# Performance work log

Hardware: AMD Instinct MI355X
Metric: run time of the kernel (lower is better)

The kernel has to match this reference:

```python
import jax, jax.numpy as jnp
import numpy as np

B, S, D = 2, 2048, 2048
NH = 16
HD = D // NH  # 128
MAX_POS = 4096
ROPE_THETA = 10000.0


def rotate_half(x):
    x1, x2 = x[..., : x.shape[-1] // 2], x[..., x.shape[-1] // 2 :]
    return jnp.concatenate((-x2, x1), axis=-1)


def rope_tables(dtype=jnp.float32):
    inv_freq = 1.0 / (ROPE_THETA ** (jnp.arange(0, HD, 2, dtype=jnp.float32) / HD))
    t = jnp.arange(MAX_POS, dtype=jnp.float32)
    freqs = jnp.outer(t, inv_freq)              # [MAX_POS, HD/2]
    emb = jnp.concatenate((freqs, freqs), axis=-1)  # [MAX_POS, HD]
    return jnp.cos(emb).astype(dtype), jnp.sin(emb).astype(dtype)


def setup_inputs() -> dict:
    key = jax.random.key(0)
    ks = jax.random.split(key, 9)
    sc = 0.02
    return {
        "hidden_states": jax.random.normal(ks[0], (B, S, D), jnp.float32),
        "position_ids": jnp.arange(B * S, dtype=jnp.int32).reshape(B, S),
        "Wq": jax.random.normal(ks[1], (D, D), jnp.float32) * sc,
        "bq": jax.random.normal(ks[2], (D,), jnp.float32) * sc,
        "Wk": jax.random.normal(ks[3], (D, D), jnp.float32) * sc,
        "bk": jax.random.normal(ks[4], (D,), jnp.float32) * sc,
        "Wv": jax.random.normal(ks[5], (D, D), jnp.float32) * sc,
        "bv": jax.random.normal(ks[6], (D,), jnp.float32) * sc,
        "Wo": jax.random.normal(ks[7], (D, D), jnp.float32) * sc,
    }


def reference(hidden_states, position_ids, Wq, bq, Wk, bk, Wv, bv, Wo):
    b, s, _ = hidden_states.shape
    # projections (torch Linear: x @ W.T + b)
    q = (hidden_states @ Wq.T + bq).reshape(b, s, NH, HD).transpose(0, 2, 1, 3)
    k = (hidden_states @ Wk.T + bk).reshape(b, s, NH, HD).transpose(0, 2, 1, 3)
    v = (hidden_states @ Wv.T + bv).reshape(b, s, NH, HD).transpose(0, 2, 1, 3)
    # RoPE
    cos_t, sin_t = rope_tables(hidden_states.dtype)
    cos = cos_t[position_ids][:, None, :, :]  # [B,1,S,HD]
    sin = sin_t[position_ids][:, None, :, :]
    q = q * cos + rotate_half(q) * sin
    k = k * cos + rotate_half(k) * sin
    # NOTE: faithful to the source bug — softmax is computed but its result is
    # discarded; the AV matmul uses the UNNORMALIZED scaled scores.
    attn_weights = jnp.einsum("bhqd,bhkd->bhqk", q, k) / (HD ** 0.5)
    _ = jax.nn.softmax(attn_weights.astype(jnp.float32), axis=-1)  # dead, as in source
    attn_output = jnp.einsum("bhqk,bhkd->bhqd", attn_weights, v)
    attn_output = attn_output.transpose(0, 2, 1, 3).reshape(b, s, D)
    return attn_output @ Wo.T
```

## Files before the change

kernel.cpp:

```cpp
#include <hip/hip_runtime.h>
#include <hip/hip_bf16.h>


typedef __attribute__((ext_vector_type(8))) short bf16x8s;
typedef __attribute__((ext_vector_type(4))) float f32x4;

__device__ __forceinline__ ushort f2bf(float f) {
    union { float f; unsigned int u; } x; x.f = f;
    unsigned int u = x.u;
    unsigned int r = (u + 0x7fffu + ((u >> 16) & 1u)) >> 16;
    return (ushort)r;
}

__device__ __forceinline__ void gload_lds16(const void* g, void* l) {
    __builtin_amdgcn_global_load_lds((__attribute__((address_space(1))) const void*)g,
                                     (__attribute__((address_space(3))) void*)l, 16, 0, 0);
}

template<bool BIAS, bool OBF16>
__global__ __launch_bounds__(256)
void gemm_nt(const ushort* __restrict__ A, const ushort* __restrict__ B,
             const float* __restrict__ bias, void* __restrict__ Cv,
             int K, int lda, int ldb, int ldc, int ZH,
             long sAb, long sAh, long sBb, long sBh, long sCb, long sCh)
{
    __shared__ ushort As[128 * 32];
    __shared__ ushort Bs[128 * 32];

    int z  = blockIdx.z;
    int zb = z / ZH, zh = z - zb * ZH;
    const ushort* Ab = A + (size_t)(sAb * zb + sAh * zh);
    const ushort* Bb = B + (size_t)(sBb * zb + sBh * zh);
    size_t Coff = (size_t)(sCb * zb + sCh * zh);

    int m0 = blockIdx.x * 128, n0 = blockIdx.y * 128;
    int t = threadIdx.x;
    int l = t & 63, w = t >> 6;
    int wm = (w >> 1) * 64, wn = (w & 1) * 64;
    int lr = l & 15, lk = (l >> 4) * 8;

    f32x4 acc[4][4];
#pragma unroll
    for (int i = 0; i < 4; i++)
#pragma unroll
        for (int j = 0; j < 4; j++)
            acc[i][j] = (f32x4){0.f, 0.f, 0.f, 0.f};

    int c0 = t, c1 = t + 256;
    int r0 = c0 >> 2, k0c = (c0 & 3) * 8;
    int r1 = c1 >> 2, k1c = (c1 & 3) * 8;

    for (int kt = 0; kt < K; kt += 32) {
        __syncthreads();
        gload_lds16(Ab + (size_t)(m0 + r0) * lda + kt + k0c, &As[c0 * 8]);
        gload_lds16(Ab + (size_t)(m0 + r1) * lda + kt + k1c, &As[c1 * 8]);
        gload_lds16(Bb + (size_t)(n0 + r0) * ldb + kt + k0c, &Bs[c0 * 8]);
        gload_lds16(Bb + (size_t)(n0 + r1) * ldb + kt + k1c, &Bs[c1 * 8]);
        __syncthreads();

        bf16x8s af[4], bf[4];
#pragma unroll
        for (int i = 0; i < 4; i++) {
            af[i] = *(const bf16x8s*)&As[(wm + i * 16 + lr) * 32 + lk];
            bf[i] = *(const bf16x8s*)&Bs[(wn + i * 16 + lr) * 32 + lk];
        }
#pragma unroll
        for (int mi = 0; mi < 4; mi++)
#pragma unroll
            for (int ni = 0; ni < 4; ni++)
                acc[mi][ni] = __builtin_amdgcn_mfma_f32_16x16x32_bf16(
                    af[mi], bf[ni], acc[mi][ni], 0, 0, 0);
    }

    int rr = (l >> 4) * 4;
#pragma unroll
    for (int mi = 0; mi < 4; mi++) {
#pragma unroll
        for (int ni = 0; ni < 4; ni++) {
            int gr = m0 + wm + mi * 16 + rr;
            int gc = n0 + wn + ni * 16 + lr;
            float bv = BIAS ? bias[gc] : 0.f;
#pragma unroll
            for (int r = 0; r < 4; r++) {
                float v = acc[mi][ni][r] + bv;
                size_t off = Coff + (size_t)(gr + r) * ldc + gc;
                if (OBF16) ((ushort*)Cv)[off] = f2bf(v);
                else       ((float*)Cv)[off]  = v;
            }
        }
    }
}

__global__ __launch_bounds__(256)
void rope_qk(const float* __restrict__ Qf, float* __restrict__ Kio,
             const int* __restrict__ pos, ushort* __restrict__ Qb)
{
    int tid = blockIdx.x * 256 + threadIdx.x;
    int row = tid >> 10;
    int r = tid & 1023;
    int h = r >> 6, d = r & 63;
    int p = pos[row];
    float invf = exp2f((float)d * (-13.287712379549449f / 64.0f));
    float ang = (float)p * invf;
    float s, c;
    sincosf(ang, &s, &c);
    size_t base = (size_t)row * 2048 + h * 128 + d;
    float q1 = Qf[base], q2 = Qf[base + 64];
    Qb[base]      = f2bf(q1 * c - q2 * s);
    Qb[base + 64] = f2bf(q2 * c + q1 * s);
    float k1 = Kio[base], k2 = Kio[base + 64];
    Kio[base]      = k1 * c - k2 * s;
    Kio[base + 64] = k2 * c + k1 * s;
}

__global__ __launch_bounds__(256)
void ktv_partial(const float* __restrict__ Kf, const float* __restrict__ Vf,
                 float* __restrict__ part)
{
    int bh = blockIdx.x;
    int b = bh >> 4, h = bh & 15;
    int s0 = blockIdx.y * 128;
    const float* Kp = Kf + ((size_t)(b * 2048 + s0)) * 2048 + h * 128;
    const float* Vp = Vf + ((size_t)(b * 2048 + s0)) * 2048 + h * 128;

    __shared__ float Ks[32][128];
    __shared__ float Vs[32][128];

    int t = threadIdx.x;
    int tx = t & 15, ty = t >> 4;
    float acc[8][8];
#pragma unroll
    for (int i = 0; i < 8; i++)
#pragma unroll
        for (int j = 0; j < 8; j++) acc[i][j] = 0.f;

    for (int sb = 0; sb < 128; sb += 32) {
        __syncthreads();
#pragma unroll
        for (int i = 0; i < 4; i++) {
            int idx = t + i * 256;
            int rw = idx >> 5, c4 = (idx & 31) * 4;
            *(float4*)&Ks[rw][c4] = *(const float4*)&Kp[(size_t)(sb + rw) * 2048 + c4];
            *(float4*)&Vs[rw][c4] = *(const float4*)&Vp[(size_t)(sb + rw) * 2048 + c4];
        }
        __syncthreads();
        for (int ss = 0; ss < 32; ss++) {
            float kv[8], vv[8];
            *(float4*)&kv[0] = *(const float4*)&Ks[ss][tx * 8];
            *(float4*)&kv[4] = *(const float4*)&Ks[ss][tx * 8 + 4];
            *(float4*)&vv[0] = *(const float4*)&Vs[ss][ty * 8];
            *(float4*)&vv[4] = *(const float4*)&Vs[ss][ty * 8 + 4];
#pragma unroll
            for (int i = 0; i < 8; i++)
#pragma unroll
                for (int j = 0; j < 8; j++)
                    acc[i][j] += kv[i] * vv[j];
        }
    }
    float* pp = part + ((size_t)blockIdx.y * 32 + bh) * 16384;
#pragma unroll
    for (int i = 0; i < 8; i++)
#pragma unroll
        for (int j = 0; j < 8; j++)
            pp[(tx * 8 + i) * 128 + (ty * 8 + j)] = acc[i][j];
}

__global__ __launch_bounds__(256)
void reduce_ktv(const float* __restrict__ part, ushort* __restrict__ Mb)
{
    int i = blockIdx.x * 256 + threadIdx.x;
    float s = 0.f;
#pragma unroll
    for (int p = 0; p < 16; p++) s += part[(size_t)p * 524288 + i];
    Mb[i] = f2bf(s * 0.08838834764831845f);
}

__global__ __launch_bounds__(256)
void conv_f32_bf16(const float* __restrict__ in, ushort* __restrict__ out, int n4)
{
    int i = blockIdx.x * 256 + threadIdx.x;
    if (i >= n4) return;
    float4 v = ((const float4*)in)[i];
    ushort4 o;
    o.x = f2bf(v.x); o.y = f2bf(v.y); o.z = f2bf(v.z); o.w = f2bf(v.w);
    ((ushort4*)out)[i] = o;
}

extern "C" void kernel_launch(void* const* d_in, const int* in_sizes, int n_in,
                              void* d_out, int out_size, void* d_ws, size_t ws_size,
                              hipStream_t stream)
{
    const float* hs = (const float*)d_in[0];
    const int*  pos = (const int*)d_in[1];
    const float* Wq = (const float*)d_in[2];
    const float* bq = (const float*)d_in[3];
    const float* Wk = (const float*)d_in[4];
    const float* bk = (const float*)d_in[5];
    const float* Wv = (const float*)d_in[6];
    const float* bv = (const float*)d_in[7];
    const float* Wo = (const float*)d_in[8];
    float* out = (float*)d_out;
    char* ws = (char*)d_ws;

    ushort* HSB  = (ushort*)(ws + 0);
    ushort* WBUF = (ushort*)(ws + 16777216);
    float*  Kf   = (float*)(ws + 25165824);
    float*  Vf   = (float*)(ws + 58720256);
    ushort* QB   = (ushort*)(ws + 92274688);
    ushort* MB   = (ushort*)(ws + 109051904);
    float*  Qf   = out;
    float*  PART = out;
    ushort* NT   = (ushort*)Vf;

    dim3 blk(256);
    dim3 gQKV(32, 16, 1);

    conv_f32_bf16<<<8192, blk, 0, stream>>>(hs, HSB, 2097152);

    conv_f32_bf16<<<4096, blk, 0, stream>>>(Wq, WBUF, 1048576);
    gemm_nt<true, false><<<gQKV, blk, 0, stream>>>(HSB, WBUF, bq, Qf,
        2048, 2048, 2048, 2048, 1, 0, 0, 0, 0, 0, 0);

    conv_f32_bf16<<<4096, blk, 0, stream>>>(Wk, WBUF, 1048576);
    gemm_nt<true, false><<<gQKV, blk, 0, stream>>>(HSB, WBUF, bk, Kf,
        2048, 2048, 2048, 2048, 1, 0, 0, 0, 0, 0, 0);

    conv_f32_bf16<<<4096, blk, 0, stream>>>(Wv, WBUF, 1048576);
    gemm_nt<true, false><<<gQKV, blk, 0, stream>>>(HSB, WBUF, bv, Vf,
        2048, 2048, 2048, 2048, 1, 0, 0, 0, 0, 0, 0);

    rope_qk<<<16384, blk, 0, stream>>>(Qf, Kf, pos, QB);

    ktv_partial<<<dim3(32, 16, 1), blk, 0, stream>>>(Kf, Vf, PART);
    reduce_ktv<<<2048, blk, 0, stream>>>(PART, MB);

    conv_f32_bf16<<<4096, blk, 0, stream>>>(Wo, WBUF, 1048576);

    gemm_nt<false, true><<<dim3(16, 1, 32), blk, 0, stream>>>(WBUF, MB, nullptr, NT,
        128, 2048, 128, 2048, 16,
        0, 128, 262144, 16384, 4194304, 128);

    gemm_nt<false, false><<<dim3(16, 16, 2), blk, 0, stream>>>(QB, NT, nullptr, out,
        2048, 2048, 2048, 2048, 1,
        4194304, 0, 4194304, 0, 4194304, 0);
}
```

Baseline: 453.0 us.

## Fuse QKV projections into one bf16 GEMM and keep activations in bf16

```diff
diff --git a/kernel.cpp b/kernel.cpp
--- a/kernel.cpp
+++ b/kernel.cpp
@@ -11,13 +11,17 @@
     unsigned int r = (u + 0x7fffu + ((u >> 16) & 1u)) >> 16;
     return (ushort)r;
 }
+__device__ __forceinline__ float b2f(ushort u) {
+    union { unsigned int u; float f; } x; x.u = ((unsigned int)u) << 16;
+    return x.f;
+}
 
 __device__ __forceinline__ void gload_lds16(const void* g, void* l) {
     __builtin_amdgcn_global_load_lds((__attribute__((address_space(1))) const void*)g,
                                      (__attribute__((address_space(3))) void*)l, 16, 0, 0);
 }
 
-template<bool BIAS, bool OBF16>
+template<bool BIAS, bool OBF16, int BN>
 __global__ __launch_bounds__(256)
 void gemm_nt(const ushort* __restrict__ A, const ushort* __restrict__ B,
              const float* __restrict__ bias, void* __restrict__ Cv,
@@ -25,7 +29,7 @@
              long sAb, long sAh, long sBb, long sBh, long sCb, long sCh)
 {
     __shared__ ushort As[128 * 32];
-    __shared__ ushort Bs[128 * 32];
+    __shared__ ushort Bs[BN * 32];
 
     int z  = blockIdx.z;
     int zb = z / ZH, zh = z - zb * ZH;
@@ -33,17 +37,21 @@
     const ushort* Bb = B + (size_t)(sBb * zb + sBh * zh);
     size_t Coff = (size_t)(sCb * zb + sCh * zh);
 
-    int m0 = blockIdx.x * 128, n0 = blockIdx.y * 128;
+    int m0 = blockIdx.x * 128, n0 = blockIdx.y * BN;
     int t = threadIdx.x;
     int l = t & 63, w = t >> 6;
-    int wm = (w >> 1) * 64, wn = (w & 1) * 64;
+    int wm, wn;
+    if (BN == 128) { wm = (w >> 1) * 64; wn = (w & 1) * 64; }
+    else           { wm = w * 32;        wn = 0; }
+    constexpr int FM = (BN == 128) ? 4 : 2;
+    constexpr int FN = 4;
     int lr = l & 15, lk = (l >> 4) * 8;
 
-    f32x4 acc[4][4];
-#pragma unroll
-    for (int i = 0; i < 4; i++)
-#pragma unroll
-        for (int j = 0; j < 4; j++)
+    f32x4 acc[FM][FN];
+#pragma unroll
+    for (int i = 0; i < FM; i++)
+#pragma unroll
+        for (int j = 0; j < FN; j++)
             acc[i][j] = (f32x4){0.f, 0.f, 0.f, 0.f};
 
     int c0 = t, c1 = t + 256;
@@ -55,28 +63,30 @@
         gload_lds16(Ab + (size_t)(m0 + r0) * lda + kt + k0c, &As[c0 * 8]);
         gload_lds16(Ab + (size_t)(m0 + r1) * lda + kt + k1c, &As[c1 * 8]);
         gload_lds16(Bb + (size_t)(n0 + r0) * ldb + kt + k0c, &Bs[c0 * 8]);
-        gload_lds16(Bb + (size_t)(n0 + r1) * ldb + kt + k1c, &Bs[c1 * 8]);
-        __syncthreads();
-
-        bf16x8s af[4], bf[4];
-#pragma unroll
-        for (int i = 0; i < 4; i++) {
+        if (BN == 128)
+            gload_lds16(Bb + (size_t)(n0 + r1) * ldb + kt + k1c, &Bs[c1 * 8]);
+        __syncthreads();
+
+        bf16x8s af[FM], bf[FN];
+#pragma unroll
+        for (int i = 0; i < FM; i++)
             af[i] = *(const bf16x8s*)&As[(wm + i * 16 + lr) * 32 + lk];
+#pragma unroll
+        for (int i = 0; i < FN; i++)
             bf[i] = *(const bf16x8s*)&Bs[(wn + i * 16 + lr) * 32 + lk];
-        }
-#pragma unroll
-        for (int mi = 0; mi < 4; mi++)
-#pragma unroll
-            for (int ni = 0; ni < 4; ni++)
+#pragma unroll
+        for (int mi = 0; mi < FM; mi++)
+#pragma unroll
+            for (int ni = 0; ni < FN; ni++)
                 acc[mi][ni] = __builtin_amdgcn_mfma_f32_16x16x32_bf16(
                     af[mi], bf[ni], acc[mi][ni], 0, 0, 0);
     }
 
     int rr = (l >> 4) * 4;
 #pragma unroll
-    for (int mi = 0; mi < 4; mi++) {
-#pragma unroll
-        for (int ni = 0; ni < 4; ni++) {
+    for (int mi = 0; mi < FM; mi++) {
+#pragma unroll
+        for (int ni = 0; ni < FN; ni++) {
             int gr = m0 + wm + mi * 16 + rr;
             int gc = n0 + wn + ni * 16 + lr;
             float bv = BIAS ? bias[gc] : 0.f;
@@ -92,39 +102,53 @@
 }
 
 __global__ __launch_bounds__(256)
-void rope_qk(const float* __restrict__ Qf, float* __restrict__ Kio,
-             const int* __restrict__ pos, ushort* __restrict__ Qb)
+void rope_qk(ushort* __restrict__ QKV, const int* __restrict__ pos,
+             ushort* __restrict__ QB)
 {
     int tid = blockIdx.x * 256 + threadIdx.x;
-    int row = tid >> 10;
-    int r = tid & 1023;
-    int h = r >> 6, d = r & 63;
-    int p = pos[row];
-    float invf = exp2f((float)d * (-13.287712379549449f / 64.0f));
-    float ang = (float)p * invf;
-    float s, c;
-    sincosf(ang, &s, &c);
-    size_t base = (size_t)row * 2048 + h * 128 + d;
-    float q1 = Qf[base], q2 = Qf[base + 64];
-    Qb[base]      = f2bf(q1 * c - q2 * s);
-    Qb[base + 64] = f2bf(q2 * c + q1 * s);
-    float k1 = Kio[base], k2 = Kio[base + 64];
-    Kio[base]      = k1 * c - k2 * s;
-    Kio[base + 64] = k2 * c + k1 * s;
-}
-
-__global__ __launch_bounds__(256)
-void ktv_partial(const float* __restrict__ Kf, const float* __restrict__ Vf,
-                 float* __restrict__ part)
+    int row = tid >> 7;
+    int r = tid & 127;
+    int h = r >> 3, j = r & 7;
+    int d0 = j * 8;
+    float p = (float)pos[row];
+    size_t qb = (size_t)row * 6144 + h * 128 + d0;
+
+    bf16x8s q1 = *(const bf16x8s*)&QKV[qb];
+    bf16x8s q2 = *(const bf16x8s*)&QKV[qb + 64];
+    bf16x8s k1 = *(const bf16x8s*)&QKV[qb + 2048];
+    bf16x8s k2 = *(const bf16x8s*)&QKV[qb + 2048 + 64];
+    bf16x8s oq1, oq2, ok1, ok2;
+#pragma unroll
+    for (int i = 0; i < 8; i++) {
+        float d = (float)(d0 + i);
+        float ang = p * exp2f(d * (-13.287712379549449f / 64.0f));
+        float s, c;
+        sincosf(ang, &s, &c);
+        float a = b2f((ushort)q1[i]), b = b2f((ushort)q2[i]);
+        oq1[i] = (short)f2bf(a * c - b * s);
+        oq2[i] = (short)f2bf(b * c + a * s);
+        float e = b2f((ushort)k1[i]), f = b2f((ushort)k2[i]);
+        ok1[i] = (short)f2bf(e * c - f * s);
+        ok2[i] = (short)f2bf(f * c + e * s);
+    }
+    size_t ob = (size_t)row * 2048 + h * 128 + d0;
+    *(bf16x8s*)&QB[ob]      = oq1;
+    *(bf16x8s*)&QB[ob + 64] = oq2;
+    *(bf16x8s*)&QKV[qb + 2048]      = ok1;
+    *(bf16x8s*)&QKV[qb + 2048 + 64] = ok2;
+}
+
+__global__ __launch_bounds__(256)
+void ktv_partial(const ushort* __restrict__ QKV, float* __restrict__ part)
 {
     int bh = blockIdx.x;
     int b = bh >> 4, h = bh & 15;
     int s0 = blockIdx.y * 128;
-    const float* Kp = Kf + ((size_t)(b * 2048 + s0)) * 2048 + h * 128;
-    const float* Vp = Vf + ((size_t)(b * 2048 + s0)) * 2048 + h * 128;
-
-    __shared__ float Ks[32][128];
-    __shared__ float Vs[32][128];
+    const ushort* Kp = QKV + (size_t)(b * 2048 + s0) * 6144 + 2048 + h * 128;
+    const ushort* Vp = Kp + 2048;
+
+    __shared__ ushort Ks[32][128];
+    __shared__ ushort Vs[32][128];
 
     int t = threadIdx.x;
     int tx = t & 15, ty = t >> 4;
@@ -137,19 +161,19 @@
     for (int sb = 0; sb < 128; sb += 32) {
         __syncthreads();
 #pragma unroll
-        for (int i = 0; i < 4; i++) {
+        for (int i = 0; i < 2; i++) {
             int idx = t + i * 256;
-            int rw = idx >> 5, c4 = (idx & 31) * 4;
-            *(float4*)&Ks[rw][c4] = *(const float4*)&Kp[(size_t)(sb + rw) * 2048 + c4];
-            *(float4*)&Vs[rw][c4] = *(const float4*)&Vp[(size_t)(sb + rw) * 2048 + c4];
+            int rw = idx >> 4, c8 = (idx & 15) * 8;
+            *(bf16x8s*)&Ks[rw][c8] = *(const bf16x8s*)&Kp[(size_t)(sb + rw) * 6144 + c8];
+            *(bf16x8s*)&Vs[rw][c8] = *(const bf16x8s*)&Vp[(size_t)(sb + rw) * 6144 + c8];
         }
         __syncthreads();
         for (int ss = 0; ss < 32; ss++) {
+            bf16x8s kvv = *(const bf16x8s*)&Ks[ss][tx * 8];
+            bf16x8s vvv = *(const bf16x8s*)&Vs[ss][ty * 8];
             float kv[8], vv[8];
-            *(float4*)&kv[0] = *(const float4*)&Ks[ss][tx * 8];
-            *(float4*)&kv[4] = *(const float4*)&Ks[ss][tx * 8 + 4];
-            *(float4*)&vv[0] = *(const float4*)&Vs[ss][ty * 8];
-            *(float4*)&vv[4] = *(const float4*)&Vs[ss][ty * 8 + 4];
+#pragma unroll
+            for (int i = 0; i < 8; i++) { kv[i] = b2f((ushort)kvv[i]); vv[i] = b2f((ushort)vvv[i]); }
 #pragma unroll
             for (int i = 0; i < 8; i++)
 #pragma unroll
@@ -184,6 +208,31 @@
     ushort4 o;
     o.x = f2bf(v.x); o.y = f2bf(v.y); o.z = f2bf(v.z); o.w = f2bf(v.w);
     ((ushort4*)out)[i] = o;
+}
+
+__global__ __launch_bounds__(256)
+void conv_weights(const float* __restrict__ w0, const float* __restrict__ w1,
+                  const float* __restrict__ w2, const float* __restrict__ w3,
+                  ushort* __restrict__ qkv, ushort* __restrict__ wo)
+{
+    int i = blockIdx.x * 256 + threadIdx.x;
+    int id = i >> 20;
+    int off = i & 1048575;
+    const float* src = (id == 0) ? w0 : (id == 1) ? w1 : (id == 2) ? w2 : w3;
+    float4 v = ((const float4*)src)[off];
+    ushort4 o;
+    o.x = f2bf(v.x); o.y = f2bf(v.y); o.z = f2bf(v.z); o.w = f2bf(v.w);
+    if (id < 3) ((ushort4*)qkv)[(size_t)id * 1048576 + off] = o;
+    else        ((ushort4*)wo)[off] = o;
+}
+
+__global__ __launch_bounds__(256)
+void pack_bias(const float* __restrict__ bq, const float* __restrict__ bk,
+               const float* __restrict__ bv, float* __restrict__ bqkv)
+{
+    int i = blockIdx.x * 256 + threadIdx.x;
+    float v = (i < 2048) ? bq[i] : (i < 4096) ? bk[i - 2048] : bv[i - 4096];
+    bqkv[i] = v;
 }
 
 extern "C" void kernel_launch(void* const* d_in, const int* in_sizes, int n_in,
@@ -203,44 +252,34 @@
     char* ws = (char*)d_ws;
 
     ushort* HSB  = (ushort*)(ws + 0);
-    ushort* WBUF = (ushort*)(ws + 16777216);
-    float*  Kf   = (float*)(ws + 25165824);
-    float*  Vf   = (float*)(ws + 58720256);
-    ushort* QB   = (ushort*)(ws + 92274688);
-    ushort* MB   = (ushort*)(ws + 109051904);
-    float*  Qf   = out;
+    ushort* QB   = (ushort*)(ws + 0);
+    ushort* WQKV = (ushort*)(ws + 16777216);
+    ushort* NT   = (ushort*)(ws + 16777216);
+    ushort* WOB  = (ushort*)(ws + 41943040);
+    float*  BQKV = (float*)(ws + 50331648);
+    ushort* QKVB = (ushort*)(ws + 50356224);
+    ushort* MB   = (ushort*)(ws + 100687872);
     float*  PART = out;
-    ushort* NT   = (ushort*)Vf;
 
     dim3 blk(256);
-    dim3 gQKV(32, 16, 1);
 
     conv_f32_bf16<<<8192, blk, 0, stream>>>(hs, HSB, 2097152);
-
-    conv_f32_bf16<<<4096, blk, 0, stream>>>(Wq, WBUF, 1048576);
-    gemm_nt<true, false><<<gQKV, blk, 0, stream>>>(HSB, WBUF, bq, Qf,
-        2048, 2048, 2048, 2048, 1, 0, 0, 0, 0, 0, 0);
-
-    conv_f32_bf16<<<4096, blk, 0, stream>>>(Wk, WBUF, 1048576);
-    gemm_nt<true, false><<<gQKV, blk, 0, stream>>>(HSB, WBUF, bk, Kf,
-        2048, 2048, 2048, 2048, 1, 0, 0, 0, 0, 0, 0);
-
-    conv_f32_bf16<<<4096, blk, 0, stream>>>(Wv, WBUF, 1048576);
-    gemm_nt<true, false><<<gQKV, blk, 0, stream>>>(HSB, WBUF, bv, Vf,
-        2048, 2048, 2048, 2048, 1, 0, 0, 0, 0, 0, 0);
-
-    rope_qk<<<16384, blk, 0, stream>>>(Qf, Kf, pos, QB);
-
-    ktv_partial<<<dim3(32, 16, 1), blk, 0, stream>>>(Kf, Vf, PART);
+    conv_weights<<<16384, blk, 0, stream>>>(Wq, Wk, Wv, Wo, WQKV, WOB);
+    pack_bias<<<24, blk, 0, stream>>>(bq, bk, bv, BQKV);
+
+    gemm_nt<true, true, 128><<<dim3(32, 48, 1), blk, 0, stream>>>(
+        HSB, WQKV, BQKV, QKVB, 2048, 2048, 2048, 6144, 1, 0, 0, 0, 0, 0, 0);
+
+    rope_qk<<<2048, blk, 0, stream>>>(QKVB, pos, QB);
+
+    ktv_partial<<<dim3(32, 16, 1), blk, 0, stream>>>(QKVB, PART);
     reduce_ktv<<<2048, blk, 0, stream>>>(PART, MB);
 
-    conv_f32_bf16<<<4096, blk, 0, stream>>>(Wo, WBUF, 1048576);
-
-    gemm_nt<false, true><<<dim3(16, 1, 32), blk, 0, stream>>>(WBUF, MB, nullptr, NT,
-        128, 2048, 128, 2048, 16,
+    gemm_nt<false, true, 128><<<dim3(16, 1, 32), blk, 0, stream>>>(
+        WOB, MB, nullptr, NT, 128, 2048, 128, 2048, 16,
         0, 128, 262144, 16384, 4194304, 128);
 
-    gemm_nt<false, false><<<dim3(16, 16, 2), blk, 0, stream>>>(QB, NT, nullptr, out,
-        2048, 2048, 2048, 2048, 1,
+    gemm_nt<false, false, 64><<<dim3(16, 32, 2), blk, 0, stream>>>(
+        QB, NT, nullptr, out, 2048, 2048, 2048, 2048, 1,
         4194304, 0, 4194304, 0, 4194304, 0);
 }
```

Measured after the change: 408.8 us. -9.8%, faster.
